# Optimization experiments

Measured on AMD Instinct MI355X. Metric: run time of the kernel, lower is better.

The kernel has to match this reference:

```python
import jax, jax.numpy as jnp
import numpy as np

HIDDEN, KEY_DIM, VALUE_DIM = 1024, 64, 64
B, T = 4, 4096


def setup_inputs() -> dict:
    key = jax.random.key(0)
    ks = jax.random.split(key, 9)
    s = 0.02
    return {
        "y_all": jax.random.normal(ks[0], (B, T, HIDDEN), dtype=jnp.float32),
        # torch nn.Linear weights: (out_features, in_features)
        "Wq": jax.random.normal(ks[1], (KEY_DIM, HIDDEN), dtype=jnp.float32) * s,
        "bq": jax.random.normal(ks[2], (KEY_DIM,), dtype=jnp.float32) * s,
        "Wk": jax.random.normal(ks[3], (KEY_DIM, HIDDEN), dtype=jnp.float32) * s,
        "bk": jax.random.normal(ks[4], (KEY_DIM,), dtype=jnp.float32) * s,
        "Wv": jax.random.normal(ks[5], (VALUE_DIM, HIDDEN), dtype=jnp.float32) * s,
        "bv": jax.random.normal(ks[6], (VALUE_DIM,), dtype=jnp.float32) * s,
        "Wo": jax.random.normal(ks[7], (HIDDEN, VALUE_DIM), dtype=jnp.float32) * s,
        "bo": jax.random.normal(ks[8], (HIDDEN,), dtype=jnp.float32) * s,
    }


def reference(y_all, Wq, bq, Wk, bk, Wv, bv, Wo, bo):
    # The original per-timestep loop is exactly causal self-attention:
    # query at position i attends over positions 0..i.
    q = jnp.einsum("bth,kh->btk", y_all, Wq) + bq          # (B,T,Dk)
    k = jnp.einsum("bth,kh->btk", y_all, Wk) + bk          # (B,T,Dk)
    v = jnp.einsum("bth,vh->btv", y_all, Wv) + bv          # (B,T,Dv)
    scale = jnp.asarray(KEY_DIM, q.dtype) ** 0.5
    scores = jnp.einsum("bqk,btk->bqt", q / scale, k)      # (B,T,T)
    t = scores.shape[-1]
    causal = jnp.tril(jnp.ones((t, t), dtype=bool))
    scores = jnp.where(causal, scores, jnp.asarray(-jnp.inf, scores.dtype))
    weights = jax.nn.softmax(scores, axis=-1)
    ctx = jnp.einsum("bqt,btv->bqv", weights, v)           # (B,T,Dv)
    out = jnp.einsum("bqv,hv->bqh", ctx, Wo) + bo          # (B,T,H)
    return out
```

## Files before the change

### kernel.cpp

```cpp
#include <hip/hip_runtime.h>


typedef __attribute__((ext_vector_type(4)))  float f32x4;
typedef __attribute__((ext_vector_type(16))) float f32x16;
typedef __attribute__((ext_vector_type(8)))  short s16x8;
typedef __attribute__((ext_vector_type(4)))  short s16x4;

#define DEV static __device__ __forceinline__

static constexpr int TT = 4096;
static constexpr int HH = 1024;
static constexpr int DD = 64;
static constexpr float MNEG = -3.0e38f;

DEV unsigned short f2bf(float f) {
  union { float f; unsigned int u; } v; v.f = f;
  unsigned int r = v.u + 0x7FFFu + ((v.u >> 16) & 1u);
  return (unsigned short)(r >> 16);
}

DEV unsigned int cvtpk(float lo, float hi) {
  unsigned int r;
  asm("v_cvt_pk_bf16_f32 %0, %1, %2" : "=v"(r) : "v"(lo), "v"(hi));
  return r;
}

DEV s16x8 mk8(unsigned int w0, unsigned int w1, unsigned int w2, unsigned int w3) {
  union { unsigned int u[4]; s16x8 v; } c;
  c.u[0] = w0; c.u[1] = w1; c.u[2] = w2; c.u[3] = w3; return c.v;
}

DEV int swzA(int row) { return ((row & 7) << 4); }
DEV int swzK(int row) { return ((row & 7) << 4) ^ ((row & 8) << 3); }

__global__ void prep_kernel(const float* __restrict__ Wq, const float* __restrict__ Wk,
                            const float* __restrict__ Wv, const float* __restrict__ Wo,
                            unsigned short* __restrict__ Wall,
                            unsigned short* __restrict__ Wo_b)
{
  int i = blockIdx.x * blockDim.x + threadIdx.x;
  int stride = gridDim.x * blockDim.x;
  const int n1 = 64 * HH;
  for (int idx = i; idx < 3 * n1; idx += stride) {
    float v = idx < n1 ? Wq[idx] : (idx < 2 * n1 ? Wk[idx - n1] : Wv[idx - 2 * n1]);
    Wall[idx] = f2bf(v);
  }
  for (int idx = i; idx < HH * DD; idx += stride) {
    int hcol = idx >> 6, d = idx & 63;
    size_t off = (size_t)(hcol >> 4) * 1024 + (d >> 5) * 512 + (hcol & 15) * 32
               + ((d >> 3) & 3) * 8 + (d & 7);
    Wo_b[off] = f2bf(Wo[idx]);
  }
}

__global__ __launch_bounds__(256, 2) void qkv_kernel(
    const float* __restrict__ y, const unsigned short* __restrict__ Wall,
    const float* __restrict__ bq, const float* __restrict__ bk,
    const float* __restrict__ bv,
    unsigned short* __restrict__ q_ws, unsigned short* __restrict__ k_ws,
    unsigned short* __restrict__ vT_ws)
{
  __shared__ unsigned short ylds[2][32 * 64];
  __shared__ unsigned short wlds[2][192 * 64];
  const int t = threadIdx.x;
  const int wv = t >> 6, lane = t & 63, g = lane >> 4, c = lane & 15;
  const int row0 = blockIdx.x * 32;
  const int bb = row0 >> 12;
  const int tb = row0 & 4095;
  const int yrow = t >> 3, ycol0 = (t & 7) * 8;

  f32x4 acc[2][3];
#pragma unroll
  for (int m = 0; m < 2; ++m)
#pragma unroll
    for (int i = 0; i < 3; ++i)
#pragma unroll
      for (int e = 0; e < 4; ++e) acc[m][i][e] = 0.0f;

  f32x4 yr[2];
  s16x8 wr[6];

  auto load_tiles = [&](int kb) {
    const float* src = y + (size_t)(row0 + yrow) * HH + kb * 64 + ycol0;
    yr[0] = *(const f32x4*)(src);
    yr[1] = *(const f32x4*)(src + 4);
#pragma unroll
    for (int ii = 0; ii < 6; ++ii) {
      int ch = t + ii * 256;
      int rw = ch >> 3, c0 = (ch & 7) * 8;
      wr[ii] = *(const s16x8*)(Wall + (size_t)rw * HH + kb * 64 + c0);
    }
  };
  auto write_tiles = [&](int buf) {
    s16x8 h0;
#pragma unroll
    for (int e = 0; e < 4; ++e) {
      h0[e]     = (short)f2bf(yr[0][e]);
      h0[e + 4] = (short)f2bf(yr[1][e]);
    }
    int byte0 = yrow * 128 + ycol0 * 2;
    *(s16x8*)((char*)ylds[buf] + (byte0 ^ swzA(yrow))) = h0;
#pragma unroll
    for (int ii = 0; ii < 6; ++ii) {
      int ch = t + ii * 256;
      int rw = ch >> 3, c0 = (ch & 7) * 8;
      int byte = rw * 128 + c0 * 2;
      *(s16x8*)((char*)wlds[buf] + (byte ^ swzA(rw))) = wr[ii];
    }
  };

  load_tiles(0);
  write_tiles(0);
  __syncthreads();
  for (int kb = 0; kb < 16; ++kb) {
    int buf = kb & 1;
    if (kb < 15) load_tiles(kb + 1);
#pragma unroll
    for (int kk = 0; kk < 2; ++kk) {
      s16x8 a[2], bfr[3];
#pragma unroll
      for (int m = 0; m < 2; ++m) {
        int ra = 16 * m + c;
        a[m] = *(const s16x8*)((char*)ylds[buf] +
                 ((ra * 128 + (kk * 32 + 8 * g) * 2) ^ swzA(ra)));
      }
#pragma unroll
      for (int i = 0; i < 3; ++i) {
        int rb = 16 * (3 * wv + i) + c;
        bfr[i] = *(const s16x8*)((char*)wlds[buf] +
                   ((rb * 128 + (kk * 32 + 8 * g) * 2) ^ swzA(rb)));
      }
#pragma unroll
      for (int m = 0; m < 2; ++m)
#pragma unroll
        for (int i = 0; i < 3; ++i)
          acc[m][i] = __builtin_amdgcn_mfma_f32_16x16x32_bf16(a[m], bfr[i], acc[m][i], 0, 0, 0);
    }
    __syncthreads();
    if (kb < 15) { write_tiles((kb + 1) & 1); __syncthreads(); }
  }

  unsigned short* elds = &wlds[0][0];
  const float qsc = 1.4426950408889634f / 8.0f;
#pragma unroll
  for (int m = 0; m < 2; ++m)
#pragma unroll
    for (int i = 0; i < 3; ++i) {
      int nt = 3 * wv + i;
      int sec = nt >> 2;
      int dcol = (nt & 3) * 16 + c;
      float bias = sec == 0 ? bq[dcol] : (sec == 1 ? bk[dcol] : bv[dcol]);
#pragma unroll
      for (int i2 = 0; i2 < 4; ++i2) {
        int rl = 16 * m + 4 * g + i2;
        float val = acc[m][i][i2] + bias;
        if (sec == 0) val *= qsc;
        if (sec < 2) elds[sec * 2048 + rl * 64 + dcol] = f2bf(val);
        else         elds[4096 + dcol * 32 + rl]       = f2bf(val);
      }
    }
  __syncthreads();
  {
    int trow = t >> 3, d0 = (t & 7) * 8;
    s16x8 vq = *(const s16x8*)(elds + trow * 64 + d0);
    s16x8 vk = *(const s16x8*)(elds + 2048 + trow * 64 + d0);
    size_t offqk = (size_t)bb * (TT * DD) + (size_t)(tb >> 5) * 2048
                 + (d0 >> 4) * 512 + trow * 16 + (d0 & 15);
    *(s16x8*)(q_ws + offqk) = vq;
    *(s16x8*)(k_ws + offqk) = vk;
    int d = t >> 2, tq = (t & 3) * 8;
    s16x8 vvv = *(const s16x8*)(elds + 4096 + d * 32 + tq);
    int tg = tb + tq;
    size_t offv = (size_t)bb * (DD * TT) + (size_t)(tg >> 6) * 4096
                + (d >> 5) * 2048 + ((tg >> 4) & 3) * 512 + (d & 31) * 16 + (tg & 15);
    *(s16x8*)(vT_ws + offv) = vvv;
  }
}

__global__ __launch_bounds__(256, 2) void attn_kernel(
    const unsigned short* __restrict__ q_ws, const unsigned short* __restrict__ k_ws,
    const unsigned short* __restrict__ vT_ws, const unsigned short* __restrict__ Wo_b,
    const float* __restrict__ bo, float* __restrict__ out)
{
  __shared__ float obuf[3 * 2048];
  __shared__ float mstat[3 * 128];
  __shared__ unsigned short clds[32 * 64];
  const int t = threadIdx.x, wv = t >> 6, lane = t & 63;
  const int qcol = lane & 31, h = lane >> 5;
  const int b = blockIdx.x & 3;
  const int jslot = blockIdx.x >> 2;
  const int j32 = (jslot < 64) ? (2 * jslot) : (127 - 2 * (jslot - 64));
  const int q0 = j32 * 32;
  const int L = j32 >> 1;
  const size_t base  = (size_t)b * TT * DD;
  const size_t vbase = (size_t)b * DD * TT;
  const int g = lane >> 4, c = lane & 15;
  const int lchunk = (lane & 31) * 16 + (lane >> 5) * 8;

  s16x8 qf[4];
  {
    const unsigned short* qp = q_ws + base + (size_t)j32 * 2048;
#pragma unroll
    for (int kk = 0; kk < 4; ++kk) qf[kk] = *(const s16x8*)(qp + kk * 512 + lchunk);
  }
  f32x16 o[2];
#pragma unroll
  for (int mt = 0; mt < 2; ++mt)
#pragma unroll
    for (int rg = 0; rg < 16; ++rg) o[mt][rg] = 0.0f;
  float m_run = MNEG, l_run = 0.0f;

  for (int kt = wv; kt <= L; kt += 4) {
    const int kv0 = kt * 64;
    s16x8 kf[2][4];
#pragma unroll
    for (int mt = 0; mt < 2; ++mt)
#pragma unroll
      for (int kk = 0; kk < 4; ++kk)
        kf[mt][kk] = *(const s16x8*)(k_ws + base +
                       (size_t)(2 * kt + mt) * 2048 + kk * 512 + lchunk);
    f32x16 s[2];
#pragma unroll
    for (int mt = 0; mt < 2; ++mt)
#pragma unroll
      for (int rg = 0; rg < 16; ++rg) s[mt][rg] = 0.0f;
    __builtin_amdgcn_s_setprio(1);
#pragma unroll
    for (int kk = 0; kk < 4; ++kk)
#pragma unroll
      for (int mt = 0; mt < 2; ++mt)
        s[mt] = __builtin_amdgcn_mfma_f32_32x32x16_bf16(kf[mt][kk], qf[kk], s[mt], 0, 0, 0);
    __builtin_amdgcn_s_setprio(0);
    s16x8 vf[2][4];
#pragma unroll
    for (int mt = 0; mt < 2; ++mt)
#pragma unroll
      for (int ks = 0; ks < 4; ++ks)
        vf[mt][ks] = *(const s16x8*)(vT_ws + vbase +
                       (size_t)kt * 4096 + mt * 2048 + ks * 512 + lchunk);
    if (kt == L) {
      int qq = q0 + qcol;
#pragma unroll
      for (int mt = 0; mt < 2; ++mt)
#pragma unroll
        for (int rg = 0; rg < 16; ++rg) {
          int kvabs = kv0 + 32 * mt + (rg & 3) + 8 * (rg >> 2) + 4 * h;
          if (kvabs > qq) s[mt][rg] = MNEG;
        }
    }
    float mx[16];
#pragma unroll
    for (int e = 0; e < 16; ++e) mx[e] = fmaxf(s[0][e], s[1][e]);
#pragma unroll
    for (int st = 8; st >= 1; st >>= 1)
#pragma unroll
      for (int e = 0; e < 8; ++e) if (e < st) mx[e] = fmaxf(mx[e], mx[e + st]);
    float pm = fmaxf(mx[0], __shfl_xor(mx[0], 32));
    float m_new;
    if (__all(pm - m_run <= 8.0f)) {
      m_new = m_run;
    } else {
      m_new = fmaxf(m_run, pm);
      float alpha = exp2f(m_run - m_new);
      l_run *= alpha;
#pragma unroll
      for (int mt = 0; mt < 2; ++mt)
#pragma unroll
        for (int rg = 0; rg < 16; ++rg) o[mt][rg] *= alpha;
      m_run = m_new;
    }
#pragma unroll
    for (int mt = 0; mt < 2; ++mt)
#pragma unroll
      for (int rg = 0; rg < 16; ++rg) s[mt][rg] = exp2f(s[mt][rg] - m_new);
    float sm[16];
#pragma unroll
    for (int e = 0; e < 16; ++e) sm[e] = s[0][e] + s[1][e];
#pragma unroll
    for (int st = 8; st >= 1; st >>= 1)
#pragma unroll
      for (int e = 0; e < 8; ++e) if (e < st) sm[e] += sm[e + st];
    float rowsum = sm[0] + __shfl_xor(sm[0], 32);
    l_run += rowsum;
    s16x8 pf[4];
#pragma unroll
    for (int mt = 0; mt < 2; ++mt) {
      unsigned int a0 = cvtpk(s[mt][0],  s[mt][1]);
      unsigned int a1 = cvtpk(s[mt][2],  s[mt][3]);
      unsigned int b0 = cvtpk(s[mt][4],  s[mt][5]);
      unsigned int b1 = cvtpk(s[mt][6],  s[mt][7]);
      unsigned int c0 = cvtpk(s[mt][8],  s[mt][9]);
      unsigned int c1 = cvtpk(s[mt][10], s[mt][11]);
      unsigned int d0 = cvtpk(s[mt][12], s[mt][13]);
      unsigned int d1 = cvtpk(s[mt][14], s[mt][15]);
      asm("v_permlane32_swap_b32 %0, %1" : "+v"(a0), "+v"(b0));
      asm("v_permlane32_swap_b32 %0, %1" : "+v"(a1), "+v"(b1));
      asm("v_permlane32_swap_b32 %0, %1" : "+v"(c0), "+v"(d0));
      asm("v_permlane32_swap_b32 %0, %1" : "+v"(c1), "+v"(d1));
      pf[2 * mt]     = mk8(a0, a1, b0, b1);
      pf[2 * mt + 1] = mk8(c0, c1, d0, d1);
    }
    __builtin_amdgcn_s_setprio(1);
#pragma unroll
    for (int ks = 0; ks < 4; ++ks)
#pragma unroll
      for (int mt = 0; mt < 2; ++mt)
        o[mt] = __builtin_amdgcn_mfma_f32_32x32x16_bf16(vf[mt][ks], pf[ks], o[mt], 0, 0, 0);
    __builtin_amdgcn_s_setprio(0);
  }

  if (wv != 0) {
#pragma unroll
    for (int mt = 0; mt < 2; ++mt)
#pragma unroll
      for (int rg = 0; rg < 16; ++rg)
        obuf[(wv - 1) * 2048 + (mt * 16 + rg) * 64 + lane] = o[mt][rg];
    mstat[(wv - 1) * 128 + lane] = m_run;
    mstat[(wv - 1) * 128 + 64 + lane] = l_run;
  }
  __syncthreads();
  if (wv == 0) {
    float mB[3], lB[3];
    float mS = m_run;
#pragma unroll
    for (int i = 0; i < 3; ++i) {
      mB[i] = mstat[i * 128 + lane];
      lB[i] = mstat[i * 128 + 64 + lane];
      mS = fmaxf(mS, mB[i]);
    }
    float f0 = exp2f(m_run - mS);
    float fi[3];
    float l_tot = l_run * f0;
#pragma unroll
    for (int i = 0; i < 3; ++i) { fi[i] = exp2f(mB[i] - mS); l_tot += lB[i] * fi[i]; }
    float inv = 1.0f / l_tot;
#pragma unroll
    for (int mt = 0; mt < 2; ++mt) {
#pragma unroll
      for (int rgq = 0; rgq < 4; ++rgq) {
        s16x4 pb;
#pragma unroll
        for (int e = 0; e < 4; ++e) {
          int rg = 4 * rgq + e;
          float val = o[mt][rg] * f0;
#pragma unroll
          for (int i = 0; i < 3; ++i)
            val += obuf[i * 2048 + (mt * 16 + rg) * 64 + lane] * fi[i];
          pb[e] = (short)f2bf(val * inv);
        }
        int d0 = 32 * mt + 8 * rgq + 4 * h;
        int byte = qcol * 128 + d0 * 2;
        *(s16x4*)((char*)clds + (byte ^ swzK(qcol))) = pb;
      }
    }
  }
  __syncthreads();

  s16x8 afr[2][2];
#pragma unroll
  for (int mt = 0; mt < 2; ++mt)
#pragma unroll
    for (int kk = 0; kk < 2; ++kk) {
      int ra = 16 * mt + c;
      afr[mt][kk] = *(const s16x8*)((char*)clds +
                      ((ra * 128 + (32 * kk + 8 * g) * 2) ^ swzK(ra)));
    }
  const int wchunk = (lane & 15) * 32 + (lane >> 4) * 8;
  const size_t orow0 = (size_t)(b * TT + q0);
#pragma unroll 4
  for (int nt = 0; nt < 16; ++nt) {
    int col = wv * 256 + 16 * nt + c;
    s16x8 bfr[2];
#pragma unroll
    for (int kk = 0; kk < 2; ++kk)
      bfr[kk] = *(const s16x8*)(Wo_b + (size_t)(wv * 16 + nt) * 1024
                                + kk * 512 + wchunk);
    f32x4 acc4[2];
#pragma unroll
    for (int mt = 0; mt < 2; ++mt)
#pragma unroll
      for (int e = 0; e < 4; ++e) acc4[mt][e] = 0.0f;
#pragma unroll
    for (int kk = 0; kk < 2; ++kk)
#pragma unroll
      for (int mt = 0; mt < 2; ++mt)
        acc4[mt] = __builtin_amdgcn_mfma_f32_16x16x32_bf16(afr[mt][kk], bfr[kk],
                                                           acc4[mt], 0, 0, 0);
    float bias = bo[col];
#pragma unroll
    for (int mt = 0; mt < 2; ++mt)
#pragma unroll
      for (int i = 0; i < 4; ++i) {
        size_t row = orow0 + 16 * mt + 4 * g + i;
        out[row * HH + col] = acc4[mt][i] + bias;
      }
  }
}

extern "C" void kernel_launch(void* const* d_in, const int* in_sizes, int n_in,
                              void* d_out, int out_size, void* d_ws, size_t ws_size,
                              hipStream_t stream)
{
  const float* y  = (const float*)d_in[0];
  const float* Wq = (const float*)d_in[1];
  const float* bq = (const float*)d_in[2];
  const float* Wk = (const float*)d_in[3];
  const float* bk = (const float*)d_in[4];
  const float* Wv = (const float*)d_in[5];
  const float* bv = (const float*)d_in[6];
  const float* Wo = (const float*)d_in[7];
  const float* bo = (const float*)d_in[8];
  float* out = (float*)d_out;
  char* ws = (char*)d_ws;
  unsigned short* Wall  = (unsigned short*)(ws);
  unsigned short* Wo_b  = (unsigned short*)(ws + 393216);
  unsigned short* q_ws  = (unsigned short*)(ws + 524288);
  unsigned short* k_ws  = (unsigned short*)(ws + 524288 + 2097152);
  unsigned short* vT_ws = (unsigned short*)(ws + 524288 + 2 * 2097152);

  prep_kernel<<<dim3(256), dim3(256), 0, stream>>>(Wq, Wk, Wv, Wo, Wall, Wo_b);
  qkv_kernel<<<dim3(512), dim3(256), 0, stream>>>(y, Wall, bq, bk, bv, q_ws, k_ws, vT_ws);
  attn_kernel<<<dim3(512), dim3(256), 0, stream>>>(q_ws, k_ws, vT_ws, Wo_b, bo, out);
}
```

Measured before the change: 58.29 us.

## Prefetch next K tile and defer softmax max/rescale after PV MFMA

The attention loop now double-buffers K fragments, issuing the next tile's K loads right after the QK MFMAs so they overlap the softmax and PV work. The online softmax is restructured so the running max is set from the first tile only, and later exponentials use that stale max. After the PV MFMA the exponentiated values are checked, and the accumulator is rescaled lazily only when they exceed 256. This takes the max reduction off the critical path between the QK and PV MFMAs, at the cost of more registers and reliance on bf16 and fp32 range headroom from the lazy rescale.

After: 57.26 us. About the same (-1.8%).

```diff
diff --git a/kernel.cpp b/kernel.cpp
--- a/kernel.cpp
+++ b/kernel.cpp
@@ -208,17 +208,20 @@
   for (int mt = 0; mt < 2; ++mt)
 #pragma unroll
     for (int rg = 0; rg < 16; ++rg) o[mt][rg] = 0.0f;
-  float m_run = MNEG, l_run = 0.0f;
-
-  for (int kt = wv; kt <= L; kt += 4) {
-    const int kv0 = kt * 64;
-    s16x8 kf[2][4];
+  float m_used = MNEG, l_run = 0.0f;
+  bool first = true;
+
+  auto loadK = [&](int kt, s16x8 (&kf)[2][4]) {
 #pragma unroll
     for (int mt = 0; mt < 2; ++mt)
 #pragma unroll
       for (int kk = 0; kk < 4; ++kk)
         kf[mt][kk] = *(const s16x8*)(k_ws + base +
                        (size_t)(2 * kt + mt) * 2048 + kk * 512 + lchunk);
+  };
+
+  auto tile = [&](int kt, s16x8 (&kf)[2][4], s16x8 (&kfn)[2][4]) {
+    const int kv0 = kt * 64;
     f32x16 s[2];
 #pragma unroll
     for (int mt = 0; mt < 2; ++mt)
@@ -231,6 +234,7 @@
       for (int mt = 0; mt < 2; ++mt)
         s[mt] = __builtin_amdgcn_mfma_f32_32x32x16_bf16(kf[mt][kk], qf[kk], s[mt], 0, 0, 0);
     __builtin_amdgcn_s_setprio(0);
+    if (kt + 4 <= L) loadK(kt + 4, kfn);
     s16x8 vf[2][4];
 #pragma unroll
     for (int mt = 0; mt < 2; ++mt)
@@ -248,40 +252,21 @@
           if (kvabs > qq) s[mt][rg] = MNEG;
         }
     }
-    float mx[16];
-#pragma unroll
-    for (int e = 0; e < 16; ++e) mx[e] = fmaxf(s[0][e], s[1][e]);
-#pragma unroll
-    for (int st = 8; st >= 1; st >>= 1)
-#pragma unroll
-      for (int e = 0; e < 8; ++e) if (e < st) mx[e] = fmaxf(mx[e], mx[e + st]);
-    float pm = fmaxf(mx[0], __shfl_xor(mx[0], 32));
-    float m_new;
-    if (__all(pm - m_run <= 8.0f)) {
-      m_new = m_run;
-    } else {
-      m_new = fmaxf(m_run, pm);
-      float alpha = exp2f(m_run - m_new);
-      l_run *= alpha;
-#pragma unroll
-      for (int mt = 0; mt < 2; ++mt)
-#pragma unroll
-        for (int rg = 0; rg < 16; ++rg) o[mt][rg] *= alpha;
-      m_run = m_new;
-    }
-#pragma unroll
-    for (int mt = 0; mt < 2; ++mt)
-#pragma unroll
-      for (int rg = 0; rg < 16; ++rg) s[mt][rg] = exp2f(s[mt][rg] - m_new);
-    float sm[16];
-#pragma unroll
-    for (int e = 0; e < 16; ++e) sm[e] = s[0][e] + s[1][e];
-#pragma unroll
-    for (int st = 8; st >= 1; st >>= 1)
-#pragma unroll
-      for (int e = 0; e < 8; ++e) if (e < st) sm[e] += sm[e + st];
-    float rowsum = sm[0] + __shfl_xor(sm[0], 32);
-    l_run += rowsum;
+    if (first) {
+      first = false;
+      float mx[16];
+#pragma unroll
+      for (int e = 0; e < 16; ++e) mx[e] = fmaxf(s[0][e], s[1][e]);
+#pragma unroll
+      for (int st = 8; st >= 1; st >>= 1)
+#pragma unroll
+        for (int e = 0; e < 8; ++e) if (e < st) mx[e] = fmaxf(mx[e], mx[e + st]);
+      m_used = fmaxf(mx[0], __shfl_xor(mx[0], 32));
+    }
+#pragma unroll
+    for (int mt = 0; mt < 2; ++mt)
+#pragma unroll
+      for (int rg = 0; rg < 16; ++rg) s[mt][rg] = exp2f(s[mt][rg] - m_used);
     s16x8 pf[4];
 #pragma unroll
     for (int mt = 0; mt < 2; ++mt) {
@@ -307,6 +292,42 @@
       for (int mt = 0; mt < 2; ++mt)
         o[mt] = __builtin_amdgcn_mfma_f32_32x32x16_bf16(vf[mt][ks], pf[ks], o[mt], 0, 0, 0);
     __builtin_amdgcn_s_setprio(0);
+    float sm[16], mxp[16];
+#pragma unroll
+    for (int e = 0; e < 16; ++e) {
+      sm[e]  = s[0][e] + s[1][e];
+      mxp[e] = fmaxf(s[0][e], s[1][e]);
+    }
+#pragma unroll
+    for (int st = 8; st >= 1; st >>= 1)
+#pragma unroll
+      for (int e = 0; e < 8; ++e)
+        if (e < st) { sm[e] += sm[e + st]; mxp[e] = fmaxf(mxp[e], mxp[e + st]); }
+    float rowsum = sm[0] + __shfl_xor(sm[0], 32);
+    float mp = fmaxf(mxp[0], __shfl_xor(mxp[0], 32));
+    l_run += rowsum;
+    if (!__all(mp <= 256.0f)) {
+      float mpc = fmaxf(mp, 1.0f);
+      float dlt = log2f(mpc);
+      float alpha = 1.0f / mpc;
+      m_used += dlt;
+      l_run *= alpha;
+#pragma unroll
+      for (int mt = 0; mt < 2; ++mt)
+#pragma unroll
+        for (int rg = 0; rg < 16; ++rg) o[mt][rg] *= alpha;
+    }
+  };
+
+  s16x8 kfA[2][4], kfB[2][4];
+  int kt = wv;
+  if (kt <= L) loadK(kt, kfA);
+  while (kt <= L) {
+    tile(kt, kfA, kfB);
+    kt += 4;
+    if (kt > L) break;
+    tile(kt, kfB, kfA);
+    kt += 4;
   }
 
   if (wv != 0) {
@@ -315,20 +336,20 @@
 #pragma unroll
       for (int rg = 0; rg < 16; ++rg)
         obuf[(wv - 1) * 2048 + (mt * 16 + rg) * 64 + lane] = o[mt][rg];
-    mstat[(wv - 1) * 128 + lane] = m_run;
+    mstat[(wv - 1) * 128 + lane] = m_used;
     mstat[(wv - 1) * 128 + 64 + lane] = l_run;
   }
   __syncthreads();
   if (wv == 0) {
     float mB[3], lB[3];
-    float mS = m_run;
+    float mS = m_used;
 #pragma unroll
     for (int i = 0; i < 3; ++i) {
       mB[i] = mstat[i * 128 + lane];
       lB[i] = mstat[i * 128 + 64 + lane];
       mS = fmaxf(mS, mB[i]);
     }
-    float f0 = exp2f(m_run - mS);
+    float f0 = exp2f(m_used - mS);
     float fi[3];
     float l_tot = l_run * f0;
 #pragma unroll
```
